# Kernel tuning notes

Measured on AMD Instinct MI355X. Metric: run time of the kernel, lower is better.

The kernel has to match this reference:

```python
import jax, jax.numpy as jnp
import numpy as np

HID = 256
OUT_DIM = 3


def _nearest_idx(c, size):
    # PyTorch grid_sample nearest, align_corners=False: idx = round(((c+1)*size-1)/2) = floor((c+1)*size/2)
    return jnp.clip(jnp.floor((c + 1.0) * size * 0.5), 0, size - 1).astype(jnp.int32)


def _mlp(x, params):
    # 4 hidden ReLU layers of 256 + linear out (LIIF imnet)
    for w, b in params[:-1]:
        x = jax.nn.relu(x @ w + b)
    w, b = params[-1]
    return x @ w + b


def setup_inputs() -> dict:
    key = jax.random.key(0)
    ks = jax.random.split(key, 16)
    B, C, H, W = 2, 64, 128, 128
    Q = 65536  # 256x256 HR queries
    feat = jax.random.normal(ks[0], (B, C, H, W), dtype=jnp.float32)
    coord = jax.random.uniform(ks[1], (B, Q, 2), dtype=jnp.float32) * 2.0 - 1.0  # in [-1,1)
    cell = jnp.full((B, Q, 2), 2.0 / 256.0, dtype=jnp.float32)
    in_dim = C * 9 + 2 + 2
    dims = [in_dim, HID, HID, HID, HID, OUT_DIM]
    inp = {"feat": feat, "coord": coord, "cell": cell}
    for i in range(5):
        fan_in = dims[i]
        inp[f"w{i}"] = jax.random.normal(ks[2 + 2 * i], (dims[i], dims[i + 1]), dtype=jnp.float32) / np.sqrt(fan_in)
        inp[f"b{i}"] = jnp.zeros((dims[i + 1],), dtype=jnp.float32)
    return inp


def reference(feat, coord, cell, w0, b0, w1, b1, w2, b2, w3, b3, w4, b4):
    params = [(w0, b0), (w1, b1), (w2, b2), (w3, b3), (w4, b4)]
    B, C, H, W = feat.shape
    dt = feat.dtype
    # feat_unfold: F.unfold(feat, 3, padding=1) -> channel order c*9 + (ki*3+kj)
    p = jnp.pad(feat, ((0, 0), (0, 0), (1, 1), (1, 1)))
    feat_u = jnp.stack([p[:, :, i:i + H, j:j + W] for i in range(3) for j in range(3)], axis=2)
    feat_flat = feat_u.reshape(B, C * 9, H * W)  # [B, 576, H*W]

    rx = 1.0 / H  # 2/H/2
    ry = 1.0 / W
    eps_shift = 1e-6
    lim = 1.0 - 1e-6
    rel_cell = cell * jnp.array([H, W], dtype=dt)

    preds, areas = [], []
    for vx in (-1.0, 1.0):
        for vy in (-1.0, 1.0):
            cx = jnp.clip(coord[..., 0] + vx * rx + eps_shift, -lim, lim)
            cy = jnp.clip(coord[..., 1] + vy * ry + eps_shift, -lim, lim)
            ix = _nearest_idx(cx, H)  # coord dim 0 -> height, grid is coord.flip(-1)
            iy = _nearest_idx(cy, W)
            lin = ix * W + iy  # [B, Q]
            q_feat = jnp.take_along_axis(feat_flat, lin[:, None, :], axis=2).transpose(0, 2, 1)  # [B,Q,576]
            # feat_coord grid-center values at the gathered cell (nearest gather of make_coord)
            qx = -1.0 + (2.0 * ix.astype(dt) + 1.0) / H
            qy = -1.0 + (2.0 * iy.astype(dt) + 1.0) / W
            rel = jnp.stack([(coord[..., 0] - qx) * H, (coord[..., 1] - qy) * W], axis=-1)  # [B,Q,2]
            mlp_in = jnp.concatenate([q_feat, rel, rel_cell], axis=-1)  # [B,Q,580]
            preds.append(_mlp(mlp_in, params))  # [B,Q,3]
            areas.append(jnp.abs(rel[..., 0] * rel[..., 1]) + 1e-9)

    # local_ensemble: swap diagonal areas
    areas[0], areas[3] = areas[3], areas[0]
    areas[1], areas[2] = areas[2], areas[1]
    tot = areas[0] + areas[1] + areas[2] + areas[3]
    ret = sum(pr * (a / tot)[..., None] for pr, a in zip(preds, areas))
    return ret
```

## Files before the change

kernel.cpp:

```cpp
#include <hip/hip_runtime.h>

typedef _Float16 half_t;
typedef _Float16 half4 __attribute__((ext_vector_type(4)));
typedef _Float16 half8 __attribute__((ext_vector_type(8)));
typedef float float4v __attribute__((ext_vector_type(4)));

#define MFMA16(a, b, c) __builtin_amdgcn_mfma_f32_16x16x32_f16(a, b, c, 0, 0, 0)

__device__ __host__ __forceinline__ int sigma_p(int s) {
  return (s & 0xC3) | ((s & 0x0C) << 2) | ((s & 0x30) >> 2);
}

__global__ __launch_bounds__(256) void pack_frags(
    const float* __restrict__ w0, const float* __restrict__ w1,
    const float* __restrict__ w2, const float* __restrict__ w3,
    const float* __restrict__ w4, half_t* __restrict__ w0p,
    half_t* __restrict__ w1p, half_t* __restrict__ w2p,
    half_t* __restrict__ w3p, half_t* __restrict__ w4p,
    half_t* __restrict__ wtp) {
  const int bb = blockIdx.x;
  const int tid = threadIdx.x;
  if (bb == 42) {
#pragma unroll
    for (int e = 0; e < 16; e++) {
      const int id = e * 256 + tid;
      const int j = id & 7;
      const int lane = (id >> 3) & 63;
      const int ks = id >> 9;
      const int n = lane & 15;
      const int k = ks * 32 + ((lane >> 4) << 3) + j;
      w4p[id] = (half_t)((n < 3) ? w4[sigma_p(k) * 3 + n] : 0.0f);
    }
#pragma unroll
    for (int e = 0; e < 4; e++)
      wtp[e * 256 + tid] = (half_t)w0[576 * 256 + e * 256 + sigma_p(tid)];
    return;
  }
  __shared__ float Wt[32][260];
  const float* w;
  half_t* out;
  int nks, ks;
  int mode;
  if (bb < 18) { w = w0; out = w0p; nks = 18; ks = bb; mode = 0; }
  else if (bb < 26) { w = w1; out = w1p; nks = 8; ks = bb - 18; mode = 1; }
  else if (bb < 34) { w = w2; out = w2p; nks = 8; ks = bb - 26; mode = 1; }
  else { w = w3; out = w3p; nks = 8; ks = bb - 34; mode = 1; }
  {
    const int n4 = (tid & 63) * 4;
    const int kr = tid >> 6;
#pragma unroll
    for (int e = 0; e < 8; e++) {
      const int kp = e * 4 + kr;
      int kg = ks * 32 + kp;
      if (mode == 0) { const int w9 = kg >> 6, c = kg & 63; kg = c * 9 + w9; }
      else kg = sigma_p(kg);
      *(float4v*)&Wt[kp][n4] = *(const float4v*)(w + (size_t)kg * 256 + n4);
    }
  }
  __syncthreads();
  const int lane = tid & 63;
  const int l15 = lane & 15;
  const int kq = (lane >> 4) << 3;
#pragma unroll
  for (int e = 0; e < 4; e++) {
    const int nt = e * 4 + (tid >> 6);
    half8 hv;
#pragma unroll
    for (int j = 0; j < 8; j++) hv[j] = (half_t)Wt[kq + j][nt * 16 + l15];
    *(half8*)&out[((nt * nks + ks) * 64 + lane) * 8] = hv;
  }
}

__global__ __launch_bounds__(256, 4) void conv_l0(
    const float* __restrict__ feat, const half_t* __restrict__ w0p,
    const float* __restrict__ b0, half_t* __restrict__ Z) {
  __shared__ alignas(16) half_t Xc[2][32][40];
  const int tid = threadIdx.x;
  const int lane = tid & 63, wave = tid >> 6, quad = lane >> 4, l15 = lane & 15;
  const int blk = blockIdx.x;
  const int b = blk >> 9;
  const int h = (blk >> 2) & 127;
  const int wbase = (blk & 3) << 5;
  const float* featB = feat + b * (64 * 128 * 128);

  auto stage = [&](int ks, int buf) {
    const int w9 = ks >> 1;
    const int di = w9 / 3;
    const int dj = w9 - 3 * di;
    const int pos = tid & 31;
    const int grp = tid >> 5;
    const int y = h + di - 1;
    const int x = wbase + pos + dj - 1;
    const bool ok = ((unsigned)y < 128u) && ((unsigned)x < 128u);
    const float* base = featB + (((ks & 1) * 32 + grp * 4) << 14) + (y << 7) + x;
    half4 hv;
#pragma unroll
    for (int u = 0; u < 4; u++) hv[u] = (half_t)(ok ? base[u << 14] : 0.0f);
    *(half4*)&Xc[buf][pos][grp * 4] = hv;
  };

  const float4v zero4 = {0.0f, 0.0f, 0.0f, 0.0f};
  float4v acc[2][4];
#pragma unroll
  for (int mt = 0; mt < 2; mt++)
#pragma unroll
    for (int jn = 0; jn < 4; jn++) acc[mt][jn] = zero4;

  stage(0, 0);
  __syncthreads();

#pragma unroll 1
  for (int ks = 0; ks < 18; ks++) {
    const int buf = ks & 1;
    half8 bw[4];
#pragma unroll
    for (int jn = 0; jn < 4; jn++)
      bw[jn] = *(const half8*)(w0p + ((((wave * 4 + jn) * 18 + ks) * 64 + lane) << 3));
    half8 a[2];
#pragma unroll
    for (int mt = 0; mt < 2; mt++)
      a[mt] = *(const half8*)(&Xc[buf][mt * 16 + l15][quad * 8]);
    if (ks + 1 < 18) {
      __syncthreads();
      stage(ks + 1, buf ^ 1);
    }
#pragma unroll
    for (int mt = 0; mt < 2; mt++)
#pragma unroll
      for (int jn = 0; jn < 4; jn++)
        acc[mt][jn] = MFMA16(bw[jn], a[mt], acc[mt][jn]);
    __syncthreads();
  }

  float4v bb[4];
#pragma unroll
  for (int jn = 0; jn < 4; jn++)
    bb[jn] = *(const float4v*)(b0 + (wave * 4 + jn) * 16 + quad * 4);
  const int posbase = b * 16384 + h * 128 + wbase;
#pragma unroll
  for (int mt = 0; mt < 2; mt++) {
    half8 o0, o1;
#pragma unroll
    for (int jn = 0; jn < 2; jn++)
#pragma unroll
      for (int rr = 0; rr < 4; rr++) {
        o0[jn * 4 + rr] = (half_t)(acc[mt][jn][rr] + bb[jn][rr]);
        o1[jn * 4 + rr] = (half_t)(acc[mt][jn + 2][rr] + bb[jn + 2][rr]);
      }
    half_t* zp = &Z[(size_t)(posbase + mt * 16 + l15) * 256 + wave * 64 + quad * 16];
    *(half8*)zp = o0;
    *(half8*)(zp + 8) = o1;
  }
}

__global__ __launch_bounds__(256, 2) void liif_main(
    const float* __restrict__ coord, const float* __restrict__ cell,
    const half_t* __restrict__ Zp, const half_t* __restrict__ wtp,
    const half_t* __restrict__ w1p, const half_t* __restrict__ w2p,
    const half_t* __restrict__ w3p, const half_t* __restrict__ w4p,
    const float* __restrict__ b1, const float* __restrict__ b2,
    const float* __restrict__ b3, const float* __restrict__ b4,
    float* __restrict__ outp) {
  __shared__ alignas(16) half_t Hs[128][280];
  __shared__ int pos4[4][64];
  __shared__ half_t relxh[4][64], relyh[4][64];
  __shared__ half_t cellxh[64], cellyh[64];
  __shared__ float area4[4][64];
  __shared__ float oacc[64][4];

  const int tid = threadIdx.x;
  const int lane = tid & 63;
  const int wave = tid >> 6;
  const int quad = lane >> 4;
  const int l15 = lane & 15;
  const int blk = blockIdx.x;
  const int batch = blk >> 10;

  {
    const int t = tid >> 6, row = tid & 63;
    const int gq = blk * 64 + row;
    const float cx0 = coord[gq * 2 + 0], cy0 = coord[gq * 2 + 1];
    const float vx = (t & 2) ? 1.0f : -1.0f;
    const float vy = (t & 1) ? 1.0f : -1.0f;
    const float r = 1.0f / 128.0f, lim = 1.0f - 1e-6f, eps = 1e-6f;
    float cx = fminf(fmaxf(cx0 + vx * r + eps, -lim), lim);
    float cy = fminf(fmaxf(cy0 + vy * r + eps, -lim), lim);
    int ix = (int)floorf((cx + 1.0f) * 64.0f);
    ix = min(max(ix, 0), 127);
    int iy = (int)floorf((cy + 1.0f) * 64.0f);
    iy = min(max(iy, 0), 127);
    float qx = -1.0f + (2.0f * ix + 1.0f) * (1.0f / 128.0f);
    float qy = -1.0f + (2.0f * iy + 1.0f) * (1.0f / 128.0f);
    float rxv = (cx0 - qx) * 128.0f;
    float ryv = (cy0 - qy) * 128.0f;
    pos4[t][row] = (batch << 14) + (ix << 7) + iy;
    relxh[t][row] = (half_t)rxv;
    relyh[t][row] = (half_t)ryv;
    area4[t][row] = fabsf(rxv * ryv) + 1e-9f;
    if (t == 0) {
      cellxh[row] = (half_t)(cell[gq * 2 + 0] * 128.0f);
      cellyh[row] = (half_t)(cell[gq * 2 + 1] * 128.0f);
      oacc[row][0] = 0.0f;
      oacc[row][1] = 0.0f;
      oacc[row][2] = 0.0f;
    }
  }
  __syncthreads();

  const float4v zero4 = {0.0f, 0.0f, 0.0f, 0.0f};
  const half8 zero8 = {0, 0, 0, 0, 0, 0, 0, 0};
  const int c8 = tid & 31;
  const int rbase = (tid >> 5) * 16;

  const half8 wt0 = *(const half8*)(wtp + 0 * 256 + c8 * 8);
  const half8 wt1 = *(const half8*)(wtp + 1 * 256 + c8 * 8);
  const half8 wt2 = *(const half8*)(wtp + 2 * 256 + c8 * 8);
  const half8 wt3 = *(const half8*)(wtp + 3 * 256 + c8 * 8);

  half8 bcur[4], bnxt[4], bf4[2];
#pragma unroll
  for (int jn = 0; jn < 4; jn++)
    bcur[jn] = *(const half8*)(w1p + ((((wave * 4 + jn) * 8 + 0) * 64 + lane) << 3));

#pragma unroll 1
  for (int p = 0; p < 2; p++) {
#pragma unroll
    for (int e = 0; e < 16; e++) {
      const int r = rbase + e;
      const int corner = 2 * p + (r >> 6);
      const int qrow = r & 63;
      const half8 z = *(const half8*)(Zp + ((size_t)pos4[corner][qrow] << 8) + c8 * 8);
      const half_t rx = relxh[corner][qrow], ry = relyh[corner][qrow];
      const half_t cx = cellxh[qrow], cy = cellyh[qrow];
      const half8 rx8 = {rx, rx, rx, rx, rx, rx, rx, rx};
      const half8 ry8 = {ry, ry, ry, ry, ry, ry, ry, ry};
      const half8 cx8 = {cx, cx, cx, cx, cx, cx, cx, cx};
      const half8 cy8 = {cy, cy, cy, cy, cy, cy, cy, cy};
      half8 v = z + rx8 * wt0 + ry8 * wt1 + cx8 * wt2 + cy8 * wt3;
      v = __builtin_elementwise_max(v, zero8);
      *(half8*)(&Hs[r][c8 * 8]) = v;
    }
    __syncthreads();

    float4v acc[8][4];
#pragma unroll 1
    for (int L = 0; L < 3; L++) {
      const half_t* wp = (L == 0) ? w1p : (L == 1) ? w2p : w3p;
      const float* bp = (L == 0) ? b1 : (L == 1) ? b2 : b3;
#pragma unroll
      for (int mt = 0; mt < 8; mt++)
#pragma unroll
        for (int jn = 0; jn < 4; jn++) acc[mt][jn] = zero4;
#pragma unroll 1
      for (int ks = 0; ks < 8; ks++) {
        if (ks + 1 < 8) {
#pragma unroll
          for (int jn = 0; jn < 4; jn++)
            bnxt[jn] =
                *(const half8*)(wp + ((((wave * 4 + jn) * 8 + ks + 1) * 64 + lane) << 3));
        }
        half8 a[8];
#pragma unroll
        for (int mt = 0; mt < 8; mt++)
          a[mt] = *(const half8*)(&Hs[mt * 16 + l15][ks * 32 + quad * 8]);
#pragma unroll
        for (int mt = 0; mt < 8; mt++)
#pragma unroll
          for (int jn = 0; jn < 4; jn++)
            acc[mt][jn] = MFMA16(bcur[jn], a[mt], acc[mt][jn]);
#pragma unroll
        for (int jn = 0; jn < 4; jn++) bcur[jn] = bnxt[jn];
      }
      __syncthreads();
      if (L < 2) {
        const half_t* wpn = (L == 0) ? w2p : w3p;
#pragma unroll
        for (int jn = 0; jn < 4; jn++)
          bcur[jn] = *(const half8*)(wpn + ((((wave * 4 + jn) * 8 + 0) * 64 + lane) << 3));
      } else {
#pragma unroll
        for (int kx = 0; kx < 2; kx++)
          bf4[kx] = *(const half8*)(w4p + (((wave * 2 + kx) * 64 + lane) << 3));
      }
      float4v bb[4];
#pragma unroll
      for (int jn = 0; jn < 4; jn++)
        bb[jn] = *(const float4v*)(bp + (wave * 4 + jn) * 16 + quad * 4);
#pragma unroll
      for (int mt = 0; mt < 8; mt++) {
        half8 o0, o1;
#pragma unroll
        for (int jn = 0; jn < 2; jn++)
#pragma unroll
          for (int rr = 0; rr < 4; rr++) {
            o0[jn * 4 + rr] = (half_t)fmaxf(acc[mt][jn][rr] + bb[jn][rr], 0.0f);
            o1[jn * 4 + rr] = (half_t)fmaxf(acc[mt][jn + 2][rr] + bb[jn + 2][rr], 0.0f);
          }
        half_t* hp = &Hs[mt * 16 + l15][wave * 64 + quad * 16];
        *(half8*)hp = o0;
        *(half8*)(hp + 8) = o1;
      }
      __syncthreads();
    }

    float4v acc4[8];
#pragma unroll
    for (int mt = 0; mt < 8; mt++) acc4[mt] = zero4;
#pragma unroll
    for (int kx = 0; kx < 2; kx++) {
      const int ks = wave * 2 + kx;
#pragma unroll
      for (int mt = 0; mt < 8; mt++) {
        half8 a = *(const half8*)(&Hs[mt * 16 + l15][ks * 32 + quad * 8]);
        acc4[mt] = MFMA16(a, bf4[kx], acc4[mt]);
      }
    }
    __syncthreads();
    float* S4f = (float*)&Hs[0][0];
    if (l15 < 4) {
#pragma unroll
      for (int mt = 0; mt < 8; mt++)
#pragma unroll
        for (int rr = 0; rr < 4; rr++)
          S4f[((wave * 128 + mt * 16 + quad * 4 + rr) << 2) + l15] = acc4[mt][rr];
    }
    __syncthreads();

    if (p == 0) {
#pragma unroll
      for (int jn = 0; jn < 4; jn++)
        bcur[jn] = *(const half8*)(w1p + ((((wave * 4 + jn) * 8 + 0) * 64 + lane) << 3));
    }

    if (tid < 192) {
      const int qrow = tid / 3;
      const int j = tid - qrow * 3;
      const int ca = 2 * p, cb = 2 * p + 1;
      float pa = b4[j] + S4f[((0 * 128 + qrow) << 2) + j] +
                 S4f[((1 * 128 + qrow) << 2) + j] + S4f[((2 * 128 + qrow) << 2) + j] +
                 S4f[((3 * 128 + qrow) << 2) + j];
      float pb = b4[j] + S4f[((0 * 128 + 64 + qrow) << 2) + j] +
                 S4f[((1 * 128 + 64 + qrow) << 2) + j] +
                 S4f[((2 * 128 + 64 + qrow) << 2) + j] +
                 S4f[((3 * 128 + 64 + qrow) << 2) + j];
      oacc[qrow][j] += pa * area4[3 - ca][qrow] + pb * area4[3 - cb][qrow];
    }
    __syncthreads();
  }

  if (tid < 192) {
    const int qrow = tid / 3;
    const int j = tid - qrow * 3;
    const float tot =
        area4[0][qrow] + area4[1][qrow] + area4[2][qrow] + area4[3][qrow];
    outp[(blk * 64 + qrow) * 3 + j] = oacc[qrow][j] / tot;
  }
}

extern "C" void kernel_launch(void* const* d_in, const int* in_sizes, int n_in,
                              void* d_out, int out_size, void* d_ws, size_t ws_size,
                              hipStream_t stream) {
  const float* feat = (const float*)d_in[0];
  const float* coord = (const float*)d_in[1];
  const float* cell = (const float*)d_in[2];
  const float* w0 = (const float*)d_in[3];
  const float* b0 = (const float*)d_in[4];
  const float* w1 = (const float*)d_in[5];
  const float* b1 = (const float*)d_in[6];
  const float* w2 = (const float*)d_in[7];
  const float* b2 = (const float*)d_in[8];
  const float* w3 = (const float*)d_in[9];
  const float* b3 = (const float*)d_in[10];
  const float* w4 = (const float*)d_in[11];
  const float* b4 = (const float*)d_in[12];

  half_t* w0p = (half_t*)d_ws;
  half_t* w1p = w0p + 147456;
  half_t* w2p = w1p + 65536;
  half_t* w3p = w2p + 65536;
  half_t* w4p = w3p + 65536;
  half_t* wtp = w4p + 4096;
  half_t* Z = (half_t*)d_ws + 524288;

  pack_frags<<<43, 256, 0, stream>>>(w0, w1, w2, w3, w4, w0p, w1p, w2p, w3p, w4p, wtp);
  conv_l0<<<1024, 256, 0, stream>>>(feat, w0p, b0, Z);
  liif_main<<<2048, 256, 0, stream>>>(coord, cell, Z, wtp, w1p, w2p, w3p, w4p, b1, b2,
                                      b3, b4, (float*)d_out);
}
```

Measured before the change: 318.5 us.

## Fuse pack, conv and MLP kernels into one persistent kernel with grid barriers

Merges the three launches (weight packing, layer-0 conv, MLP) into a single persistent kernel of 512 blocks that synchronises phases with atomic grid barriers. The conv phase now covers 64 positions per block instead of 32, and the MLP phase loops over query tiles in a grid-stride loop. The aim is to remove launch gaps and tail effects between kernels. In exchange it needs a memset for the counter and depends on all 512 blocks being co-resident; if they are not, the barrier deadlocks, and the fixed block count may lower occupancy in the MLP phase.

```diff
diff --git a/kernel.cpp b/kernel.cpp
--- a/kernel.cpp
+++ b/kernel.cpp
@@ -11,201 +11,171 @@
   return (s & 0xC3) | ((s & 0x0C) << 2) | ((s & 0x30) >> 2);
 }
 
-__global__ __launch_bounds__(256) void pack_frags(
-    const float* __restrict__ w0, const float* __restrict__ w1,
-    const float* __restrict__ w2, const float* __restrict__ w3,
-    const float* __restrict__ w4, half_t* __restrict__ w0p,
+struct SmemA { float Wt[32][260]; };
+struct SmemB { alignas(16) half_t Xc[2][64][40]; };
+struct SmemC {
+  alignas(16) half_t Hs[128][280];
+  int pos4[4][64];
+  half_t relxh[4][64], relyh[4][64];
+  half_t cellxh[64], cellyh[64];
+  float area4[4][64];
+  float oacc[64][4];
+};
+
+__device__ __forceinline__ void grid_barrier(int* cnt, int target) {
+  __syncthreads();
+  if (threadIdx.x == 0) {
+    __hip_atomic_fetch_add(cnt, 1, __ATOMIC_ACQ_REL, __HIP_MEMORY_SCOPE_AGENT);
+    while (__hip_atomic_load(cnt, __ATOMIC_ACQUIRE, __HIP_MEMORY_SCOPE_AGENT) <
+           target) {
+      __builtin_amdgcn_s_sleep(8);
+    }
+  }
+  __syncthreads();
+}
+
+__global__ __launch_bounds__(256, 2) void liif_fused(
+    const float* __restrict__ feat, const float* __restrict__ coord,
+    const float* __restrict__ cell, const float* __restrict__ w0,
+    const float* __restrict__ w1, const float* __restrict__ w2,
+    const float* __restrict__ w3, const float* __restrict__ w4,
+    const float* __restrict__ b0, const float* __restrict__ b1,
+    const float* __restrict__ b2, const float* __restrict__ b3,
+    const float* __restrict__ b4, half_t* __restrict__ w0p,
     half_t* __restrict__ w1p, half_t* __restrict__ w2p,
     half_t* __restrict__ w3p, half_t* __restrict__ w4p,
-    half_t* __restrict__ wtp) {
-  const int bb = blockIdx.x;
-  const int tid = threadIdx.x;
-  if (bb == 42) {
-#pragma unroll
-    for (int e = 0; e < 16; e++) {
-      const int id = e * 256 + tid;
-      const int j = id & 7;
-      const int lane = (id >> 3) & 63;
-      const int ks = id >> 9;
-      const int n = lane & 15;
-      const int k = ks * 32 + ((lane >> 4) << 3) + j;
-      w4p[id] = (half_t)((n < 3) ? w4[sigma_p(k) * 3 + n] : 0.0f);
-    }
-#pragma unroll
-    for (int e = 0; e < 4; e++)
-      wtp[e * 256 + tid] = (half_t)w0[576 * 256 + e * 256 + sigma_p(tid)];
-    return;
-  }
-  __shared__ float Wt[32][260];
-  const float* w;
-  half_t* out;
-  int nks, ks;
-  int mode;
-  if (bb < 18) { w = w0; out = w0p; nks = 18; ks = bb; mode = 0; }
-  else if (bb < 26) { w = w1; out = w1p; nks = 8; ks = bb - 18; mode = 1; }
-  else if (bb < 34) { w = w2; out = w2p; nks = 8; ks = bb - 26; mode = 1; }
-  else { w = w3; out = w3p; nks = 8; ks = bb - 34; mode = 1; }
-  {
-    const int n4 = (tid & 63) * 4;
-    const int kr = tid >> 6;
-#pragma unroll
-    for (int e = 0; e < 8; e++) {
-      const int kp = e * 4 + kr;
-      int kg = ks * 32 + kp;
-      if (mode == 0) { const int w9 = kg >> 6, c = kg & 63; kg = c * 9 + w9; }
-      else kg = sigma_p(kg);
-      *(float4v*)&Wt[kp][n4] = *(const float4v*)(w + (size_t)kg * 256 + n4);
-    }
-  }
-  __syncthreads();
-  const int lane = tid & 63;
-  const int l15 = lane & 15;
-  const int kq = (lane >> 4) << 3;
-#pragma unroll
-  for (int e = 0; e < 4; e++) {
-    const int nt = e * 4 + (tid >> 6);
-    half8 hv;
-#pragma unroll
-    for (int j = 0; j < 8; j++) hv[j] = (half_t)Wt[kq + j][nt * 16 + l15];
-    *(half8*)&out[((nt * nks + ks) * 64 + lane) * 8] = hv;
-  }
-}
-
-__global__ __launch_bounds__(256, 4) void conv_l0(
-    const float* __restrict__ feat, const half_t* __restrict__ w0p,
-    const float* __restrict__ b0, half_t* __restrict__ Z) {
-  __shared__ alignas(16) half_t Xc[2][32][40];
-  const int tid = threadIdx.x;
-  const int lane = tid & 63, wave = tid >> 6, quad = lane >> 4, l15 = lane & 15;
-  const int blk = blockIdx.x;
-  const int b = blk >> 9;
-  const int h = (blk >> 2) & 127;
-  const int wbase = (blk & 3) << 5;
-  const float* featB = feat + b * (64 * 128 * 128);
-
-  auto stage = [&](int ks, int buf) {
-    const int w9 = ks >> 1;
-    const int di = w9 / 3;
-    const int dj = w9 - 3 * di;
-    const int pos = tid & 31;
-    const int grp = tid >> 5;
-    const int y = h + di - 1;
-    const int x = wbase + pos + dj - 1;
-    const bool ok = ((unsigned)y < 128u) && ((unsigned)x < 128u);
-    const float* base = featB + (((ks & 1) * 32 + grp * 4) << 14) + (y << 7) + x;
-    half4 hv;
-#pragma unroll
-    for (int u = 0; u < 4; u++) hv[u] = (half_t)(ok ? base[u << 14] : 0.0f);
-    *(half4*)&Xc[buf][pos][grp * 4] = hv;
-  };
-
-  const float4v zero4 = {0.0f, 0.0f, 0.0f, 0.0f};
-  float4v acc[2][4];
-#pragma unroll
-  for (int mt = 0; mt < 2; mt++)
-#pragma unroll
-    for (int jn = 0; jn < 4; jn++) acc[mt][jn] = zero4;
-
-  stage(0, 0);
-  __syncthreads();
-
-#pragma unroll 1
-  for (int ks = 0; ks < 18; ks++) {
-    const int buf = ks & 1;
-    half8 bw[4];
-#pragma unroll
-    for (int jn = 0; jn < 4; jn++)
-      bw[jn] = *(const half8*)(w0p + ((((wave * 4 + jn) * 18 + ks) * 64 + lane) << 3));
-    half8 a[2];
-#pragma unroll
-    for (int mt = 0; mt < 2; mt++)
-      a[mt] = *(const half8*)(&Xc[buf][mt * 16 + l15][quad * 8]);
-    if (ks + 1 < 18) {
-      __syncthreads();
-      stage(ks + 1, buf ^ 1);
-    }
-#pragma unroll
-    for (int mt = 0; mt < 2; mt++)
-#pragma unroll
-      for (int jn = 0; jn < 4; jn++)
-        acc[mt][jn] = MFMA16(bw[jn], a[mt], acc[mt][jn]);
-    __syncthreads();
-  }
-
-  float4v bb[4];
-#pragma unroll
-  for (int jn = 0; jn < 4; jn++)
-    bb[jn] = *(const float4v*)(b0 + (wave * 4 + jn) * 16 + quad * 4);
-  const int posbase = b * 16384 + h * 128 + wbase;
-#pragma unroll
-  for (int mt = 0; mt < 2; mt++) {
-    half8 o0, o1;
-#pragma unroll
-    for (int jn = 0; jn < 2; jn++)
-#pragma unroll
-      for (int rr = 0; rr < 4; rr++) {
-        o0[jn * 4 + rr] = (half_t)(acc[mt][jn][rr] + bb[jn][rr]);
-        o1[jn * 4 + rr] = (half_t)(acc[mt][jn + 2][rr] + bb[jn + 2][rr]);
-      }
-    half_t* zp = &Z[(size_t)(posbase + mt * 16 + l15) * 256 + wave * 64 + quad * 16];
-    *(half8*)zp = o0;
-    *(half8*)(zp + 8) = o1;
-  }
-}
-
-__global__ __launch_bounds__(256, 2) void liif_main(
-    const float* __restrict__ coord, const float* __restrict__ cell,
-    const half_t* __restrict__ Zp, const half_t* __restrict__ wtp,
-    const half_t* __restrict__ w1p, const half_t* __restrict__ w2p,
-    const half_t* __restrict__ w3p, const half_t* __restrict__ w4p,
-    const float* __restrict__ b1, const float* __restrict__ b2,
-    const float* __restrict__ b3, const float* __restrict__ b4,
+    half_t* __restrict__ wtp, half_t* __restrict__ Z, int* __restrict__ sync,
     float* __restrict__ outp) {
-  __shared__ alignas(16) half_t Hs[128][280];
-  __shared__ int pos4[4][64];
-  __shared__ half_t relxh[4][64], relyh[4][64];
-  __shared__ half_t cellxh[64], cellyh[64];
-  __shared__ float area4[4][64];
-  __shared__ float oacc[64][4];
-
+  __shared__ union { SmemA a; SmemB b; SmemC c; } smem;
   const int tid = threadIdx.x;
   const int lane = tid & 63;
   const int wave = tid >> 6;
   const int quad = lane >> 4;
   const int l15 = lane & 15;
-  const int blk = blockIdx.x;
-  const int batch = blk >> 10;
+  const int bid = blockIdx.x;
+
+  if (bid == 42) {
+#pragma unroll
+    for (int e = 0; e < 16; e++) {
+      const int id = e * 256 + tid;
+      const int j = id & 7;
+      const int ln = (id >> 3) & 63;
+      const int ks = id >> 9;
+      const int n = ln & 15;
+      const int k = ks * 32 + ((ln >> 4) << 3) + j;
+      w4p[id] = (half_t)((n < 3) ? w4[sigma_p(k) * 3 + n] : 0.0f);
+    }
+#pragma unroll
+    for (int e = 0; e < 4; e++)
+      wtp[e * 256 + tid] = (half_t)w0[576 * 256 + e * 256 + sigma_p(tid)];
+  } else if (bid < 42) {
+    const float* w;
+    half_t* out;
+    int nks, ks, mode;
+    if (bid < 18) { w = w0; out = w0p; nks = 18; ks = bid; mode = 0; }
+    else if (bid < 26) { w = w1; out = w1p; nks = 8; ks = bid - 18; mode = 1; }
+    else if (bid < 34) { w = w2; out = w2p; nks = 8; ks = bid - 26; mode = 1; }
+    else { w = w3; out = w3p; nks = 8; ks = bid - 34; mode = 1; }
+    {
+      const int n4 = (tid & 63) * 4;
+      const int kr = tid >> 6;
+#pragma unroll
+      for (int e = 0; e < 8; e++) {
+        const int kp = e * 4 + kr;
+        int kg = ks * 32 + kp;
+        if (mode == 0) { const int w9 = kg >> 6, c = kg & 63; kg = c * 9 + w9; }
+        else kg = sigma_p(kg);
+        *(float4v*)&smem.a.Wt[kp][n4] = *(const float4v*)(w + (size_t)kg * 256 + n4);
+      }
+    }
+    __syncthreads();
+    const int kq = (lane >> 4) << 3;
+#pragma unroll
+    for (int e = 0; e < 4; e++) {
+      const int nt = e * 4 + (tid >> 6);
+      half8 hv;
+#pragma unroll
+      for (int j = 0; j < 8; j++) hv[j] = (half_t)smem.a.Wt[kq + j][nt * 16 + l15];
+      *(half8*)&out[((nt * nks + ks) * 64 + lane) * 8] = hv;
+    }
+  }
+  grid_barrier(sync, 512);
 
   {
-    const int t = tid >> 6, row = tid & 63;
-    const int gq = blk * 64 + row;
-    const float cx0 = coord[gq * 2 + 0], cy0 = coord[gq * 2 + 1];
-    const float vx = (t & 2) ? 1.0f : -1.0f;
-    const float vy = (t & 1) ? 1.0f : -1.0f;
-    const float r = 1.0f / 128.0f, lim = 1.0f - 1e-6f, eps = 1e-6f;
-    float cx = fminf(fmaxf(cx0 + vx * r + eps, -lim), lim);
-    float cy = fminf(fmaxf(cy0 + vy * r + eps, -lim), lim);
-    int ix = (int)floorf((cx + 1.0f) * 64.0f);
-    ix = min(max(ix, 0), 127);
-    int iy = (int)floorf((cy + 1.0f) * 64.0f);
-    iy = min(max(iy, 0), 127);
-    float qx = -1.0f + (2.0f * ix + 1.0f) * (1.0f / 128.0f);
-    float qy = -1.0f + (2.0f * iy + 1.0f) * (1.0f / 128.0f);
-    float rxv = (cx0 - qx) * 128.0f;
-    float ryv = (cy0 - qy) * 128.0f;
-    pos4[t][row] = (batch << 14) + (ix << 7) + iy;
-    relxh[t][row] = (half_t)rxv;
-    relyh[t][row] = (half_t)ryv;
-    area4[t][row] = fabsf(rxv * ryv) + 1e-9f;
-    if (t == 0) {
-      cellxh[row] = (half_t)(cell[gq * 2 + 0] * 128.0f);
-      cellyh[row] = (half_t)(cell[gq * 2 + 1] * 128.0f);
-      oacc[row][0] = 0.0f;
-      oacc[row][1] = 0.0f;
-      oacc[row][2] = 0.0f;
+    const int b = bid >> 8;
+    const int h = (bid >> 1) & 127;
+    const int wbase = (bid & 1) << 6;
+    const float* featB = feat + b * (64 * 128 * 128);
+
+    auto stage = [&](int ks, int buf) {
+      const int w9 = ks >> 1;
+      const int di = w9 / 3;
+      const int dj = w9 - 3 * di;
+      const int pos = tid & 63;
+      const int grp = tid >> 6;
+      const int y = h + di - 1;
+      const int x = wbase + pos + dj - 1;
+      const bool ok = ((unsigned)y < 128u) && ((unsigned)x < 128u);
+      const float* base = featB + (((ks & 1) * 32 + grp * 8) << 14) + (y << 7) + x;
+      half4 h0, h1;
+#pragma unroll
+      for (int u = 0; u < 4; u++) h0[u] = (half_t)(ok ? base[u << 14] : 0.0f);
+#pragma unroll
+      for (int u = 0; u < 4; u++) h1[u] = (half_t)(ok ? base[(u + 4) << 14] : 0.0f);
+      *(half4*)&smem.b.Xc[buf][pos][grp * 8] = h0;
+      *(half4*)&smem.b.Xc[buf][pos][grp * 8 + 4] = h1;
+    };
+
+    const float4v zero4 = {0.0f, 0.0f, 0.0f, 0.0f};
+    float4v acc[4][4];
+#pragma unroll
+    for (int mt = 0; mt < 4; mt++)
+#pragma unroll
+      for (int jn = 0; jn < 4; jn++) acc[mt][jn] = zero4;
+
+    stage(0, 0);
+    __syncthreads();
+#pragma unroll 1
+    for (int ks = 0; ks < 18; ks++) {
+      const int buf = ks & 1;
+      if (ks + 1 < 18) stage(ks + 1, buf ^ 1);
+      half8 bw[4];
+#pragma unroll
+      for (int jn = 0; jn < 4; jn++)
+        bw[jn] = *(const half8*)(w0p + ((((wave * 4 + jn) * 18 + ks) * 64 + lane) << 3));
+      half8 a[4];
+#pragma unroll
+      for (int mt = 0; mt < 4; mt++)
+        a[mt] = *(const half8*)(&smem.b.Xc[buf][mt * 16 + l15][quad * 8]);
+#pragma unroll
+      for (int mt = 0; mt < 4; mt++)
+#pragma unroll
+        for (int jn = 0; jn < 4; jn++)
+          acc[mt][jn] = MFMA16(bw[jn], a[mt], acc[mt][jn]);
+      __syncthreads();
+    }
+
+    float4v bb[4];
+#pragma unroll
+    for (int jn = 0; jn < 4; jn++)
+      bb[jn] = *(const float4v*)(b0 + (wave * 4 + jn) * 16 + quad * 4);
+    const int posbase = b * 16384 + h * 128 + wbase;
+#pragma unroll
+    for (int mt = 0; mt < 4; mt++) {
+      half8 o0, o1;
+#pragma unroll
+      for (int jn = 0; jn < 2; jn++)
+#pragma unroll
+        for (int rr = 0; rr < 4; rr++) {
+          o0[jn * 4 + rr] = (half_t)(acc[mt][jn][rr] + bb[jn][rr]);
+          o1[jn * 4 + rr] = (half_t)(acc[mt][jn + 2][rr] + bb[jn + 2][rr]);
+        }
+      half_t* zp = &Z[(size_t)(posbase + mt * 16 + l15) * 256 + wave * 64 + quad * 16];
+      *(half8*)zp = o0;
+      *(half8*)(zp + 8) = o1;
     }
   }
-  __syncthreads();
+  grid_barrier(sync, 1024);
 
   const float4v zero4 = {0.0f, 0.0f, 0.0f, 0.0f};
   const half8 zero8 = {0, 0, 0, 0, 0, 0, 0, 0};
@@ -223,137 +193,175 @@
     bcur[jn] = *(const half8*)(w1p + ((((wave * 4 + jn) * 8 + 0) * 64 + lane) << 3));
 
 #pragma unroll 1
-  for (int p = 0; p < 2; p++) {
-#pragma unroll
-    for (int e = 0; e < 16; e++) {
-      const int r = rbase + e;
-      const int corner = 2 * p + (r >> 6);
-      const int qrow = r & 63;
-      const half8 z = *(const half8*)(Zp + ((size_t)pos4[corner][qrow] << 8) + c8 * 8);
-      const half_t rx = relxh[corner][qrow], ry = relyh[corner][qrow];
-      const half_t cx = cellxh[qrow], cy = cellyh[qrow];
-      const half8 rx8 = {rx, rx, rx, rx, rx, rx, rx, rx};
-      const half8 ry8 = {ry, ry, ry, ry, ry, ry, ry, ry};
-      const half8 cx8 = {cx, cx, cx, cx, cx, cx, cx, cx};
-      const half8 cy8 = {cy, cy, cy, cy, cy, cy, cy, cy};
-      half8 v = z + rx8 * wt0 + ry8 * wt1 + cx8 * wt2 + cy8 * wt3;
-      v = __builtin_elementwise_max(v, zero8);
-      *(half8*)(&Hs[r][c8 * 8]) = v;
-    }
+  for (int tile = bid; tile < 2048; tile += 512) {
+    const int batch = tile >> 10;
     __syncthreads();
 
-    float4v acc[8][4];
-#pragma unroll 1
-    for (int L = 0; L < 3; L++) {
-      const half_t* wp = (L == 0) ? w1p : (L == 1) ? w2p : w3p;
-      const float* bp = (L == 0) ? b1 : (L == 1) ? b2 : b3;
-#pragma unroll
-      for (int mt = 0; mt < 8; mt++)
-#pragma unroll
-        for (int jn = 0; jn < 4; jn++) acc[mt][jn] = zero4;
-#pragma unroll 1
-      for (int ks = 0; ks < 8; ks++) {
-        if (ks + 1 < 8) {
+    {
+      const int t = tid >> 6, row = tid & 63;
+      const int gq = tile * 64 + row;
+      const float cx0 = coord[gq * 2 + 0], cy0 = coord[gq * 2 + 1];
+      const float vx = (t & 2) ? 1.0f : -1.0f;
+      const float vy = (t & 1) ? 1.0f : -1.0f;
+      const float r = 1.0f / 128.0f, lim = 1.0f - 1e-6f, eps = 1e-6f;
+      float cx = fminf(fmaxf(cx0 + vx * r + eps, -lim), lim);
+      float cy = fminf(fmaxf(cy0 + vy * r + eps, -lim), lim);
+      int ix = (int)floorf((cx + 1.0f) * 64.0f);
+      ix = min(max(ix, 0), 127);
+      int iy = (int)floorf((cy + 1.0f) * 64.0f);
+      iy = min(max(iy, 0), 127);
+      float qx = -1.0f + (2.0f * ix + 1.0f) * (1.0f / 128.0f);
+      float qy = -1.0f + (2.0f * iy + 1.0f) * (1.0f / 128.0f);
+      float rxv = (cx0 - qx) * 128.0f;
+      float ryv = (cy0 - qy) * 128.0f;
+      smem.c.pos4[t][row] = (batch << 14) + (ix << 7) + iy;
+      smem.c.relxh[t][row] = (half_t)rxv;
+      smem.c.relyh[t][row] = (half_t)ryv;
+      smem.c.area4[t][row] = fabsf(rxv * ryv) + 1e-9f;
+      if (t == 0) {
+        smem.c.cellxh[row] = (half_t)(cell[gq * 2 + 0] * 128.0f);
+        smem.c.cellyh[row] = (half_t)(cell[gq * 2 + 1] * 128.0f);
+        smem.c.oacc[row][0] = 0.0f;
+        smem.c.oacc[row][1] = 0.0f;
+        smem.c.oacc[row][2] = 0.0f;
+      }
+    }
+    __syncthreads();
+
+#pragma unroll 1
+    for (int p = 0; p < 2; p++) {
+#pragma unroll
+      for (int e = 0; e < 16; e++) {
+        const int r = rbase + e;
+        const int corner = 2 * p + (r >> 6);
+        const int qrow = r & 63;
+        const half8 z =
+            *(const half8*)(Z + ((size_t)smem.c.pos4[corner][qrow] << 8) + c8 * 8);
+        const half_t rx = smem.c.relxh[corner][qrow], ry = smem.c.relyh[corner][qrow];
+        const half_t cx = smem.c.cellxh[qrow], cy = smem.c.cellyh[qrow];
+        const half8 rx8 = {rx, rx, rx, rx, rx, rx, rx, rx};
+        const half8 ry8 = {ry, ry, ry, ry, ry, ry, ry, ry};
+        const half8 cx8 = {cx, cx, cx, cx, cx, cx, cx, cx};
+        const half8 cy8 = {cy, cy, cy, cy, cy, cy, cy, cy};
+        half8 v = z + rx8 * wt0 + ry8 * wt1 + cx8 * wt2 + cy8 * wt3;
+        v = __builtin_elementwise_max(v, zero8);
+        *(half8*)(&smem.c.Hs[r][c8 * 8]) = v;
+      }
+      __syncthreads();
+
+      float4v acc[8][4];
+#pragma unroll 1
+      for (int L = 0; L < 3; L++) {
+        const half_t* wp = (L == 0) ? w1p : (L == 1) ? w2p : w3p;
+        const float* bp = (L == 0) ? b1 : (L == 1) ? b2 : b3;
+#pragma unroll
+        for (int mt = 0; mt < 8; mt++)
+#pragma unroll
+          for (int jn = 0; jn < 4; jn++) acc[mt][jn] = zero4;
+#pragma unroll 1
+        for (int ks = 0; ks < 8; ks++) {
+          if (ks + 1 < 8) {
+#pragma unroll
+            for (int jn = 0; jn < 4; jn++)
+              bnxt[jn] = *(const half8*)(wp +
+                                         ((((wave * 4 + jn) * 8 + ks + 1) * 64 + lane) << 3));
+          }
+          half8 a[8];
+#pragma unroll
+          for (int mt = 0; mt < 8; mt++)
+            a[mt] = *(const half8*)(&smem.c.Hs[mt * 16 + l15][ks * 32 + quad * 8]);
+#pragma unroll
+          for (int mt = 0; mt < 8; mt++)
+#pragma unroll
+            for (int jn = 0; jn < 4; jn++)
+              acc[mt][jn] = MFMA16(bcur[jn], a[mt], acc[mt][jn]);
+#pragma unroll
+          for (int jn = 0; jn < 4; jn++) bcur[jn] = bnxt[jn];
+        }
+        __syncthreads();
+        if (L < 2) {
+          const half_t* wpn = (L == 0) ? w2p : w3p;
 #pragma unroll
           for (int jn = 0; jn < 4; jn++)
-            bnxt[jn] =
-                *(const half8*)(wp + ((((wave * 4 + jn) * 8 + ks + 1) * 64 + lane) << 3));
-        }
-        half8 a[8];
+            bcur[jn] =
+                *(const half8*)(wpn + ((((wave * 4 + jn) * 8 + 0) * 64 + lane) << 3));
+        } else {
+#pragma unroll
+          for (int kx = 0; kx < 2; kx++)
+            bf4[kx] = *(const half8*)(w4p + (((wave * 2 + kx) * 64 + lane) << 3));
+        }
+        float4v bb[4];
+#pragma unroll
+        for (int jn = 0; jn < 4; jn++)
+          bb[jn] = *(const float4v*)(bp + (wave * 4 + jn) * 16 + quad * 4);
+#pragma unroll
+        for (int mt = 0; mt < 8; mt++) {
+          half8 o0, o1;
+#pragma unroll
+          for (int jn = 0; jn < 2; jn++)
+#pragma unroll
+            for (int rr = 0; rr < 4; rr++) {
+              o0[jn * 4 + rr] = (half_t)fmaxf(acc[mt][jn][rr] + bb[jn][rr], 0.0f);
+              o1[jn * 4 + rr] = (half_t)fmaxf(acc[mt][jn + 2][rr] + bb[jn + 2][rr], 0.0f);
+            }
+          half_t* hp = &smem.c.Hs[mt * 16 + l15][wave * 64 + quad * 16];
+          *(half8*)hp = o0;
+          *(half8*)(hp + 8) = o1;
+        }
+        __syncthreads();
+      }
+
+      float4v acc4[8];
+#pragma unroll
+      for (int mt = 0; mt < 8; mt++) acc4[mt] = zero4;
+#pragma unroll
+      for (int kx = 0; kx < 2; kx++) {
+        const int ks = wave * 2 + kx;
+#pragma unroll
+        for (int mt = 0; mt < 8; mt++) {
+          half8 a = *(const half8*)(&smem.c.Hs[mt * 16 + l15][ks * 32 + quad * 8]);
+          acc4[mt] = MFMA16(a, bf4[kx], acc4[mt]);
+        }
+      }
+      __syncthreads();
+      float* S4f = (float*)&smem.c.Hs[0][0];
+      if (l15 < 4) {
 #pragma unroll
         for (int mt = 0; mt < 8; mt++)
-          a[mt] = *(const half8*)(&Hs[mt * 16 + l15][ks * 32 + quad * 8]);
-#pragma unroll
-        for (int mt = 0; mt < 8; mt++)
-#pragma unroll
-          for (int jn = 0; jn < 4; jn++)
-            acc[mt][jn] = MFMA16(bcur[jn], a[mt], acc[mt][jn]);
-#pragma unroll
-        for (int jn = 0; jn < 4; jn++) bcur[jn] = bnxt[jn];
-      }
-      __syncthreads();
-      if (L < 2) {
-        const half_t* wpn = (L == 0) ? w2p : w3p;
-#pragma unroll
-        for (int jn = 0; jn < 4; jn++)
-          bcur[jn] = *(const half8*)(wpn + ((((wave * 4 + jn) * 8 + 0) * 64 + lane) << 3));
-      } else {
-#pragma unroll
-        for (int kx = 0; kx < 2; kx++)
-          bf4[kx] = *(const half8*)(w4p + (((wave * 2 + kx) * 64 + lane) << 3));
-      }
-      float4v bb[4];
-#pragma unroll
-      for (int jn = 0; jn < 4; jn++)
-        bb[jn] = *(const float4v*)(bp + (wave * 4 + jn) * 16 + quad * 4);
-#pragma unroll
-      for (int mt = 0; mt < 8; mt++) {
-        half8 o0, o1;
-#pragma unroll
-        for (int jn = 0; jn < 2; jn++)
-#pragma unroll
-          for (int rr = 0; rr < 4; rr++) {
-            o0[jn * 4 + rr] = (half_t)fmaxf(acc[mt][jn][rr] + bb[jn][rr], 0.0f);
-            o1[jn * 4 + rr] = (half_t)fmaxf(acc[mt][jn + 2][rr] + bb[jn + 2][rr], 0.0f);
-          }
-        half_t* hp = &Hs[mt * 16 + l15][wave * 64 + quad * 16];
-        *(half8*)hp = o0;
-        *(half8*)(hp + 8) = o1;
-      }
-      __syncthreads();
-    }
-
-    float4v acc4[8];
-#pragma unroll
-    for (int mt = 0; mt < 8; mt++) acc4[mt] = zero4;
-#pragma unroll
-    for (int kx = 0; kx < 2; kx++) {
-      const int ks = wave * 2 + kx;
-#pragma unroll
-      for (int mt = 0; mt < 8; mt++) {
-        half8 a = *(const half8*)(&Hs[mt * 16 + l15][ks * 32 + quad * 8]);
-        acc4[mt] = MFMA16(a, bf4[kx], acc4[mt]);
-      }
-    }
-    __syncthreads();
-    float* S4f = (float*)&Hs[0][0];
-    if (l15 < 4) {
-#pragma unroll
-      for (int mt = 0; mt < 8; mt++)
-#pragma unroll
-        for (int rr = 0; rr < 4; rr++)
-          S4f[((wave * 128 + mt * 16 + quad * 4 + rr) << 2) + l15] = acc4[mt][rr];
-    }
-    __syncthreads();
-
-    if (p == 0) {
+#pragma unroll
+          for (int rr = 0; rr < 4; rr++)
+            S4f[((wave * 128 + mt * 16 + quad * 4 + rr) << 2) + l15] = acc4[mt][rr];
+      }
+      __syncthreads();
+
 #pragma unroll
       for (int jn = 0; jn < 4; jn++)
         bcur[jn] = *(const half8*)(w1p + ((((wave * 4 + jn) * 8 + 0) * 64 + lane) << 3));
+
+      if (tid < 192) {
+        const int qrow = tid / 3;
+        const int j = tid - qrow * 3;
+        const int ca = 2 * p, cb = 2 * p + 1;
+        float pa = b4[j] + S4f[((0 * 128 + qrow) << 2) + j] +
+                   S4f[((1 * 128 + qrow) << 2) + j] + S4f[((2 * 128 + qrow) << 2) + j] +
+                   S4f[((3 * 128 + qrow) << 2) + j];
+        float pb = b4[j] + S4f[((0 * 128 + 64 + qrow) << 2) + j] +
+                   S4f[((1 * 128 + 64 + qrow) << 2) + j] +
+                   S4f[((2 * 128 + 64 + qrow) << 2) + j] +
+                   S4f[((3 * 128 + 64 + qrow) << 2) + j];
+        smem.c.oacc[qrow][j] +=
+            pa * smem.c.area4[3 - ca][qrow] + pb * smem.c.area4[3 - cb][qrow];
+      }
+      __syncthreads();
     }
 
     if (tid < 192) {
       const int qrow = tid / 3;
       const int j = tid - qrow * 3;
-      const int ca = 2 * p, cb = 2 * p + 1;
-      float pa = b4[j] + S4f[((0 * 128 + qrow) << 2) + j] +
-                 S4f[((1 * 128 + qrow) << 2) + j] + S4f[((2 * 128 + qrow) << 2) + j] +
-                 S4f[((3 * 128 + qrow) << 2) + j];
-      float pb = b4[j] + S4f[((0 * 128 + 64 + qrow) << 2) + j] +
-                 S4f[((1 * 128 + 64 + qrow) << 2) + j] +
-                 S4f[((2 * 128 + 64 + qrow) << 2) + j] +
-                 S4f[((3 * 128 + 64 + qrow) << 2) + j];
-      oacc[qrow][j] += pa * area4[3 - ca][qrow] + pb * area4[3 - cb][qrow];
-    }
-    __syncthreads();
-  }
-
-  if (tid < 192) {
-    const int qrow = tid / 3;
-    const int j = tid - qrow * 3;
-    const float tot =
-        area4[0][qrow] + area4[1][qrow] + area4[2][qrow] + area4[3][qrow];
-    outp[(blk * 64 + qrow) * 3 + j] = oacc[qrow][j] / tot;
+      const float tot = smem.c.area4[0][qrow] + smem.c.area4[1][qrow] +
+                        smem.c.area4[2][qrow] + smem.c.area4[3][qrow];
+      outp[(tile * 64 + qrow) * 3 + j] = smem.c.oacc[qrow][j] / tot;
+    }
   }
 }
 
@@ -381,9 +389,11 @@
   half_t* w4p = w3p + 65536;
   half_t* wtp = w4p + 4096;
   half_t* Z = (half_t*)d_ws + 524288;
-
-  pack_frags<<<43, 256, 0, stream>>>(w0, w1, w2, w3, w4, w0p, w1p, w2p, w3p, w4p, wtp);
-  conv_l0<<<1024, 256, 0, stream>>>(feat, w0p, b0, Z);
-  liif_main<<<2048, 256, 0, stream>>>(coord, cell, Z, wtp, w1p, w2p, w3p, w4p, b1, b2,
-                                      b3, b4, (float*)d_out);
+  int* sync = (int*)((char*)d_ws + (size_t)(524288 + 8388608) * 2);
+  float* outp = (float*)d_out;
+
+  hipMemsetAsync(sync, 0, 64, stream);
+  liif_fused<<<512, 256, 0, stream>>>(feat, coord, cell, w0, w1, w2, w3, w4, b0,
+                                      b1, b2, b3, b4, w0p, w1p, w2p, w3p, w4p,
+                                      wtp, Z, sync, outp);
 }
```

After: 478.1 us. 1.5x slower.

## Stage full 3x34 input halo once in conv_l0 and fold weight packing into it

Applied to the files above, without the earlier changes.

conv_l0 now loads the whole 3-row by 34-column by 64-channel feature halo into shared memory once, then reads all nine shifted taps from it. Before, each of the 18 k-steps restaged strided global reads behind two barriers per step. The packing of w1..w4 and wtp moves into extra blocks appended to the conv_l0 grid, so pack_frags shrinks to a w0-only kernel. This removes per-step synchronisation and repeated global traffic, at the cost of more shared memory per block and some uneven extra blocks in the conv grid.

```diff
diff --git a/kernel.cpp b/kernel.cpp
--- a/kernel.cpp
+++ b/kernel.cpp
@@ -11,50 +11,21 @@
   return (s & 0xC3) | ((s & 0x0C) << 2) | ((s & 0x30) >> 2);
 }
 
-__global__ __launch_bounds__(256) void pack_frags(
-    const float* __restrict__ w0, const float* __restrict__ w1,
-    const float* __restrict__ w2, const float* __restrict__ w3,
-    const float* __restrict__ w4, half_t* __restrict__ w0p,
-    half_t* __restrict__ w1p, half_t* __restrict__ w2p,
-    half_t* __restrict__ w3p, half_t* __restrict__ w4p,
-    half_t* __restrict__ wtp) {
-  const int bb = blockIdx.x;
+__global__ __launch_bounds__(256) void pack_w0(const float* __restrict__ w0,
+                                               half_t* __restrict__ w0p) {
+  __shared__ float Wt[32][260];
+  const int ks = blockIdx.x;
   const int tid = threadIdx.x;
-  if (bb == 42) {
-#pragma unroll
-    for (int e = 0; e < 16; e++) {
-      const int id = e * 256 + tid;
-      const int j = id & 7;
-      const int lane = (id >> 3) & 63;
-      const int ks = id >> 9;
-      const int n = lane & 15;
-      const int k = ks * 32 + ((lane >> 4) << 3) + j;
-      w4p[id] = (half_t)((n < 3) ? w4[sigma_p(k) * 3 + n] : 0.0f);
-    }
-#pragma unroll
-    for (int e = 0; e < 4; e++)
-      wtp[e * 256 + tid] = (half_t)w0[576 * 256 + e * 256 + sigma_p(tid)];
-    return;
-  }
-  __shared__ float Wt[32][260];
-  const float* w;
-  half_t* out;
-  int nks, ks;
-  int mode;
-  if (bb < 18) { w = w0; out = w0p; nks = 18; ks = bb; mode = 0; }
-  else if (bb < 26) { w = w1; out = w1p; nks = 8; ks = bb - 18; mode = 1; }
-  else if (bb < 34) { w = w2; out = w2p; nks = 8; ks = bb - 26; mode = 1; }
-  else { w = w3; out = w3p; nks = 8; ks = bb - 34; mode = 1; }
   {
     const int n4 = (tid & 63) * 4;
     const int kr = tid >> 6;
 #pragma unroll
     for (int e = 0; e < 8; e++) {
       const int kp = e * 4 + kr;
-      int kg = ks * 32 + kp;
-      if (mode == 0) { const int w9 = kg >> 6, c = kg & 63; kg = c * 9 + w9; }
-      else kg = sigma_p(kg);
-      *(float4v*)&Wt[kp][n4] = *(const float4v*)(w + (size_t)kg * 256 + n4);
+      const int kg = ks * 32 + kp;
+      const int w9 = kg >> 6, c = kg & 63;
+      const int kgo = c * 9 + w9;
+      *(float4v*)&Wt[kp][n4] = *(const float4v*)(w0 + (size_t)kgo * 256 + n4);
     }
   }
   __syncthreads();
@@ -67,51 +38,118 @@
     half8 hv;
 #pragma unroll
     for (int j = 0; j < 8; j++) hv[j] = (half_t)Wt[kq + j][nt * 16 + l15];
-    *(half8*)&out[((nt * nks + ks) * 64 + lane) * 8] = hv;
+    *(half8*)&w0p[((nt * 18 + ks) * 64 + lane) * 8] = hv;
   }
 }
 
 __global__ __launch_bounds__(256, 4) void conv_l0(
     const float* __restrict__ feat, const half_t* __restrict__ w0p,
-    const float* __restrict__ b0, half_t* __restrict__ Z) {
-  __shared__ alignas(16) half_t Xc[2][32][40];
+    const float* __restrict__ b0, half_t* __restrict__ Z,
+    const float* __restrict__ w1, const float* __restrict__ w2,
+    const float* __restrict__ w3, const float* __restrict__ w4,
+    const float* __restrict__ w0, half_t* __restrict__ w1p,
+    half_t* __restrict__ w2p, half_t* __restrict__ w3p,
+    half_t* __restrict__ w4p, half_t* __restrict__ wtp) {
+  __shared__ union {
+    half_t Ft[3 * 34 * 72];
+    float Wt[32][260];
+  } sm;
   const int tid = threadIdx.x;
   const int lane = tid & 63, wave = tid >> 6, quad = lane >> 4, l15 = lane & 15;
-  const int blk = blockIdx.x;
-  const int b = blk >> 9;
-  const int h = (blk >> 2) & 127;
-  const int wbase = (blk & 3) << 5;
+  const int bid = blockIdx.x;
+
+  if (bid >= 1024) {
+    const int bb = bid - 1006;
+    if (bb == 42) {
+#pragma unroll
+      for (int e = 0; e < 16; e++) {
+        const int id = e * 256 + tid;
+        const int j = id & 7;
+        const int ln = (id >> 3) & 63;
+        const int ks = id >> 9;
+        const int n = ln & 15;
+        const int k = ks * 32 + ((ln >> 4) << 3) + j;
+        w4p[id] = (half_t)((n < 3) ? w4[sigma_p(k) * 3 + n] : 0.0f);
+      }
+#pragma unroll
+      for (int e = 0; e < 4; e++)
+        wtp[e * 256 + tid] = (half_t)w0[576 * 256 + e * 256 + sigma_p(tid)];
+      return;
+    }
+    const float* w;
+    half_t* out;
+    int ks;
+    if (bb < 26) { w = w1; out = w1p; ks = bb - 18; }
+    else if (bb < 34) { w = w2; out = w2p; ks = bb - 26; }
+    else { w = w3; out = w3p; ks = bb - 34; }
+    {
+      const int n4 = (tid & 63) * 4;
+      const int kr = tid >> 6;
+#pragma unroll
+      for (int e = 0; e < 8; e++) {
+        const int kp = e * 4 + kr;
+        const int kg = sigma_p(ks * 32 + kp);
+        *(float4v*)&sm.Wt[kp][n4] = *(const float4v*)(w + (size_t)kg * 256 + n4);
+      }
+    }
+    __syncthreads();
+    const int kq = (lane >> 4) << 3;
+#pragma unroll
+    for (int e = 0; e < 4; e++) {
+      const int nt = e * 4 + (tid >> 6);
+      half8 hv;
+#pragma unroll
+      for (int j = 0; j < 8; j++) hv[j] = (half_t)sm.Wt[kq + j][nt * 16 + l15];
+      *(half8*)&out[((nt * 8 + ks) * 64 + lane) * 8] = hv;
+    }
+    return;
+  }
+
+  const int b = bid >> 9;
+  const int h = (bid >> 2) & 127;
+  const int wbase = (bid & 3) << 5;
   const float* featB = feat + b * (64 * 128 * 128);
 
-  auto stage = [&](int ks, int buf) {
+#pragma unroll
+  for (int it = 0; it < 24; it++) {
+    const int r = it * 8 + wave * 2 + (lane >> 5);
+    const int xi = lane & 31;
+    const int di = r >> 6, c = r & 63;
+    const int y = h + di - 1;
+    const int x = wbase + xi - 1;
+    float v = 0.0f;
+    if ((unsigned)y < 128u && (unsigned)x < 128u) v = featB[(c << 14) + (y << 7) + x];
+    sm.Ft[(di * 34 + xi) * 72 + c] = (half_t)v;
+  }
+#pragma unroll
+  for (int e = 0; e < 2; e++) {
+    const int id2 = e * 256 + tid;
+    if (id2 < 384) {
+      const int r = id2 >> 1;
+      const int xi = 32 + (id2 & 1);
+      const int di = r >> 6, c = r & 63;
+      const int y = h + di - 1;
+      const int x = wbase + xi - 1;
+      float v = 0.0f;
+      if ((unsigned)y < 128u && (unsigned)x < 128u) v = featB[(c << 14) + (y << 7) + x];
+      sm.Ft[(di * 34 + xi) * 72 + c] = (half_t)v;
+    }
+  }
+  __syncthreads();
+
+  const float4v zero4 = {0.0f, 0.0f, 0.0f, 0.0f};
+  float4v acc[2][4];
+#pragma unroll
+  for (int mt = 0; mt < 2; mt++)
+#pragma unroll
+    for (int jn = 0; jn < 4; jn++) acc[mt][jn] = zero4;
+
+#pragma unroll 1
+  for (int ks = 0; ks < 18; ks++) {
     const int w9 = ks >> 1;
     const int di = w9 / 3;
     const int dj = w9 - 3 * di;
-    const int pos = tid & 31;
-    const int grp = tid >> 5;
-    const int y = h + di - 1;
-    const int x = wbase + pos + dj - 1;
-    const bool ok = ((unsigned)y < 128u) && ((unsigned)x < 128u);
-    const float* base = featB + (((ks & 1) * 32 + grp * 4) << 14) + (y << 7) + x;
-    half4 hv;
-#pragma unroll
-    for (int u = 0; u < 4; u++) hv[u] = (half_t)(ok ? base[u << 14] : 0.0f);
-    *(half4*)&Xc[buf][pos][grp * 4] = hv;
-  };
-
-  const float4v zero4 = {0.0f, 0.0f, 0.0f, 0.0f};
-  float4v acc[2][4];
-#pragma unroll
-  for (int mt = 0; mt < 2; mt++)
-#pragma unroll
-    for (int jn = 0; jn < 4; jn++) acc[mt][jn] = zero4;
-
-  stage(0, 0);
-  __syncthreads();
-
-#pragma unroll 1
-  for (int ks = 0; ks < 18; ks++) {
-    const int buf = ks & 1;
+    const int ch = ((ks & 1) << 5) + quad * 8;
     half8 bw[4];
 #pragma unroll
     for (int jn = 0; jn < 4; jn++)
@@ -119,23 +157,18 @@
     half8 a[2];
 #pragma unroll
     for (int mt = 0; mt < 2; mt++)
-      a[mt] = *(const half8*)(&Xc[buf][mt * 16 + l15][quad * 8]);
-    if (ks + 1 < 18) {
-      __syncthreads();
-      stage(ks + 1, buf ^ 1);
-    }
+      a[mt] = *(const half8*)&sm.Ft[(di * 34 + mt * 16 + l15 + dj) * 72 + ch];
 #pragma unroll
     for (int mt = 0; mt < 2; mt++)
 #pragma unroll
       for (int jn = 0; jn < 4; jn++)
         acc[mt][jn] = MFMA16(bw[jn], a[mt], acc[mt][jn]);
-    __syncthreads();
-  }
-
-  float4v bb[4];
+  }
+
+  float4v bb4[4];
 #pragma unroll
   for (int jn = 0; jn < 4; jn++)
-    bb[jn] = *(const float4v*)(b0 + (wave * 4 + jn) * 16 + quad * 4);
+    bb4[jn] = *(const float4v*)(b0 + (wave * 4 + jn) * 16 + quad * 4);
   const int posbase = b * 16384 + h * 128 + wbase;
 #pragma unroll
   for (int mt = 0; mt < 2; mt++) {
@@ -144,8 +177,8 @@
     for (int jn = 0; jn < 2; jn++)
 #pragma unroll
       for (int rr = 0; rr < 4; rr++) {
-        o0[jn * 4 + rr] = (half_t)(acc[mt][jn][rr] + bb[jn][rr]);
-        o1[jn * 4 + rr] = (half_t)(acc[mt][jn + 2][rr] + bb[jn + 2][rr]);
+        o0[jn * 4 + rr] = (half_t)(acc[mt][jn][rr] + bb4[jn][rr]);
+        o1[jn * 4 + rr] = (half_t)(acc[mt][jn + 2][rr] + bb4[jn + 2][rr]);
       }
     half_t* zp = &Z[(size_t)(posbase + mt * 16 + l15) * 256 + wave * 64 + quad * 16];
     *(half8*)zp = o0;
@@ -382,8 +415,9 @@
   half_t* wtp = w4p + 4096;
   half_t* Z = (half_t*)d_ws + 524288;
 
-  pack_frags<<<43, 256, 0, stream>>>(w0, w1, w2, w3, w4, w0p, w1p, w2p, w3p, w4p, wtp);
-  conv_l0<<<1024, 256, 0, stream>>>(feat, w0p, b0, Z);
-  liif_main<<<2048, 256, 0, stream>>>(coord, cell, Z, wtp, w1p, w2p, w3p, w4p, b1, b2,
-                                      b3, b4, (float*)d_out);
+  pack_w0<<<18, 256, 0, stream>>>(w0, w0p);
+  conv_l0<<<1049, 256, 0, stream>>>(feat, w0p, b0, Z, w1, w2, w3, w4, w0, w1p,
+                                    w2p, w3p, w4p, wtp);
+  liif_main<<<2048, 256, 0, stream>>>(coord, cell, Z, wtp, w1p, w2p, w3p, w4p,
+                                      b1, b2, b3, b4, (float*)d_out);
 }
```

New measurement: 315.2 us. Within noise of the previous version (-1.0%).
